# Performance work log

Measured on AMD Instinct MI355X. Metric: run time of the kernel, lower is better.

The kernel has to match this reference:

```python
import jax, jax.numpy as jnp
import numpy as np

C = 512
NUM_GROUPS = 32
EPS = 1e-6


def setup_inputs() -> dict:
    key = jax.random.key(0)
    ks = jax.random.split(key, 6)
    B, H, W = 4, 64, 64
    x = jax.random.normal(ks[0], (B, H, W, C), dtype=jnp.float32)
    # GroupNorm affine params (flax default init: scale=1, bias=0)
    gn_scale = jnp.ones((C,), jnp.float32)
    gn_bias = jnp.zeros((C,), jnp.float32)
    # 1x1 convs == per-pixel dense layers; weight [C_in, C_out], bias [C_out]
    def dense(k):
        return jax.random.normal(k, (C, C), dtype=jnp.float32) * 0.02
    wq, wk, wv, wo = dense(ks[1]), dense(ks[2]), dense(ks[3]), dense(ks[4])
    bq = jnp.zeros((C,), jnp.float32)
    bk = jnp.zeros((C,), jnp.float32)
    bv = jnp.zeros((C,), jnp.float32)
    bo = jnp.zeros((C,), jnp.float32)
    return {"x": x, "gn_scale": gn_scale, "gn_bias": gn_bias,
            "wq": wq, "bq": bq, "wk": wk, "bk": bk,
            "wv": wv, "bv": bv, "wo": wo, "bo": bo}


def _group_norm(x, scale, bias):
    B, H, W, Cc = x.shape
    g = NUM_GROUPS
    xg = x.reshape(B, H, W, g, Cc // g)
    mean = jnp.mean(xg, axis=(1, 2, 4), keepdims=True)
    var = jnp.var(xg, axis=(1, 2, 4), keepdims=True)
    xn = (xg - mean) * jax.lax.rsqrt(var + EPS)
    xn = xn.reshape(B, H, W, Cc)
    return xn * scale + bias


def reference(x, gn_scale, gn_bias, wq, bq, wk, bk, wv, bv, wo, bo):
    B, H, W, Cc = x.shape
    hn = _group_norm(x, gn_scale, gn_bias)
    # 1x1 convs
    q = (hn @ wq + bq).reshape(B, H * W, Cc)
    k = (hn @ wk + bk).reshape(B, H * W, Cc)
    v = (hn @ wv + bv).reshape(B, H * W, Cc)
    scale = jnp.asarray(Cc, x.dtype) ** -0.5
    # scores[b,i,j] = <q_i, k_j> * c^-0.5; softmax over keys j
    attn = jax.nn.softmax(jnp.einsum('bic,bjc->bij', q, k) * scale, axis=-1)
    out = jnp.einsum('bij,bjc->bic', attn, v).reshape(B, H, W, Cc)
    return x + (out @ wo + bo)
```

## Files before the change

### kernel.cpp

```cpp
#include <hip/hip_runtime.h>


typedef __attribute__((ext_vector_type(8))) __bf16 bf16x8;
typedef __attribute__((ext_vector_type(4))) __bf16 bf16x4;
typedef __attribute__((ext_vector_type(4))) float  floatx4;

#define C_DIM 512
#define SPB   4096
#define MTOT  16384

#define HN_OFF  ((size_t)0)
#define Q_OFF   ((size_t)16 << 20)
#define K_OFF   ((size_t)32 << 20)
#define V4_OFF  ((size_t)48 << 20)
#define WT_OFF  ((size_t)64 << 20)
#define O1_OFF  ((size_t)68 << 20)
#define ML_OFF  ((size_t)84 << 20)
#define GS_OFF  (ML_OFF + (size_t)(256 << 10))

__device__ inline floatx4 mfma16(bf16x8 a, bf16x8 b, floatx4 c) {
    return __builtin_amdgcn_mfma_f32_16x16x32_bf16(a, b, c, 0, 0, 0);
}

__device__ inline void gload16(const void* g, void* lds) {
    __builtin_amdgcn_global_load_lds(
        (const __attribute__((address_space(1))) unsigned int*)g,
        (__attribute__((address_space(3))) unsigned int*)lds, 16, 0, 0);
}

__global__ __launch_bounds__(256) void zero_stats(float* gstats) {
    gstats[threadIdx.x] = 0.f;
}

__global__ __launch_bounds__(256) void gn_stats(
    const float* __restrict__ x, float* __restrict__ gstats) {
    int bg = blockIdx.x;
    int b = bg >> 5, g = bg & 31;
    int tid = threadIdx.x;
    int cq = tid & 3, s0 = tid >> 2;
    const float* base = x + (size_t)b * SPB * C_DIM + g * 16 + cq * 4
                          + (size_t)blockIdx.y * 1024 * C_DIM;
    float sum = 0.f, sq = 0.f;
#pragma unroll 4
    for (int i = 0; i < 16; ++i) {
        floatx4 v = *(const floatx4*)(base + (size_t)(i * 64 + s0) * C_DIM);
        sum += v[0] + v[1] + v[2] + v[3];
        sq  += v[0]*v[0] + v[1]*v[1] + v[2]*v[2] + v[3]*v[3];
    }
#pragma unroll
    for (int off = 1; off < 64; off <<= 1) {
        sum += __shfl_xor(sum, off);
        sq  += __shfl_xor(sq,  off);
    }
    __shared__ float sm[8];
    int w = tid >> 6, lane = tid & 63;
    if (lane == 0) { sm[w] = sum; sm[4 + w] = sq; }
    __syncthreads();
    if (tid == 0) {
        atomicAdd(&gstats[bg * 2],     sm[0] + sm[1] + sm[2] + sm[3]);
        atomicAdd(&gstats[bg * 2 + 1], sm[4] + sm[5] + sm[6] + sm[7]);
    }
}

__global__ __launch_bounds__(256) void gn_apply(
    const float* __restrict__ x, const float* __restrict__ gstats,
    const float* __restrict__ gsc, const float* __restrict__ gbi,
    __bf16* __restrict__ hn) {
    int bg = blockIdx.x;
    int b = bg >> 5, g = bg & 31;
    int tid = threadIdx.x;
    int cq = tid & 3, s0 = tid >> 2;
    float S  = gstats[bg * 2], Qs = gstats[bg * 2 + 1];
    float mean = S * (1.f / 65536.f);
    float var  = Qs * (1.f / 65536.f) - mean * mean;
    float rstd = rsqrtf(var + 1e-6f);
    float sc[4], bi[4];
#pragma unroll
    for (int j = 0; j < 4; ++j) {
        float s_ = gsc[g * 16 + cq * 4 + j] * rstd;
        sc[j] = s_;
        bi[j] = gbi[g * 16 + cq * 4 + j] - mean * s_;
    }
    size_t off = (size_t)b * SPB * C_DIM + g * 16 + cq * 4
               + (size_t)blockIdx.y * 1024 * C_DIM;
    const float* base = x + off;
    __bf16* hbase = hn + off;
#pragma unroll 4
    for (int i = 0; i < 16; ++i) {
        floatx4 v = *(const floatx4*)(base + (size_t)(i * 64 + s0) * C_DIM);
        bf16x4 o;
#pragma unroll
        for (int j = 0; j < 4; ++j) o[j] = (__bf16)(v[j] * sc[j] + bi[j]);
        *(bf16x4*)(hbase + (size_t)(i * 64 + s0) * C_DIM) = o;
    }
}

__global__ __launch_bounds__(256) void wt_kernel(
    const float* __restrict__ w0, const float* __restrict__ w1,
    const float* __restrict__ w2, const float* __restrict__ w3,
    __bf16* __restrict__ wt) {
    const float* srcs[4] = {w0, w1, w2, w3};
    const float* src = srcs[blockIdx.z];
    __bf16* dst = wt + (size_t)blockIdx.z * C_DIM * C_DIM;
    __shared__ float tile[32][33];
    int tx = threadIdx.x & 31, ty = threadIdx.x >> 5;
    int gx = blockIdx.x * 32, gy = blockIdx.y * 32;
#pragma unroll
    for (int i = 0; i < 4; ++i)
        tile[ty + i * 8][tx] = src[(size_t)(gy + ty + i * 8) * C_DIM + gx + tx];
    __syncthreads();
#pragma unroll
    for (int i = 0; i < 4; ++i) {
        int n = gx + ty + i * 8;
        int k = gy + tx;
        dst[(size_t)n * C_DIM + k] = (__bf16)tile[tx][ty + i * 8];
    }
}

__global__ __launch_bounds__(256, 2) void proj_qkv(
    const __bf16* __restrict__ hn, const __bf16* __restrict__ wt_all,
    const float* __restrict__ bq, const float* __restrict__ bk,
    const float* __restrict__ bv, __bf16* __restrict__ qout,
    __bf16* __restrict__ kout, __bf16* __restrict__ v4out) {
    int z = blockIdx.z;
    const __bf16* wt = wt_all + (size_t)z * C_DIM * C_DIM;
    const float* bias = (z == 0) ? bq : (z == 1) ? bk : bv;
    __shared__ __bf16 Alds[128 * 32];
    __shared__ __bf16 Blds[128 * 32];
    int tid = threadIdx.x, lane = tid & 63, w = tid >> 6;
    int c = lane & 15, quad = lane >> 4;
    int wm = w & 1, wn = w >> 1;
    int mbase = blockIdx.x * 128, nbase = blockIdx.y * 128;
    floatx4 acc[4][4] = {};
    for (int kb = 0; kb < 16; ++kb) {
        __syncthreads();
#pragma unroll
        for (int p = 0; p < 2; ++p) {
            int chunk0 = w * 128 + p * 64;
            int chunk = chunk0 + lane;
            int row = chunk >> 2, qk = chunk & 3;
            gload16(hn + (size_t)(mbase + row) * C_DIM + kb * 32 + qk * 8, Alds + chunk0 * 8);
            gload16(wt + (size_t)(nbase + row) * C_DIM + kb * 32 + qk * 8, Blds + chunk0 * 8);
        }
        __syncthreads();
        bf16x8 af[4], bfr[4];
#pragma unroll
        for (int mt = 0; mt < 4; ++mt)
            af[mt] = *(const bf16x8*)(Alds + (wm * 64 + mt * 16 + c) * 32 + quad * 8);
#pragma unroll
        for (int nt = 0; nt < 4; ++nt)
            bfr[nt] = *(const bf16x8*)(Blds + (wn * 64 + nt * 16 + c) * 32 + quad * 8);
#pragma unroll
        for (int mt = 0; mt < 4; ++mt)
#pragma unroll
            for (int nt = 0; nt < 4; ++nt)
                acc[mt][nt] = mfma16(af[mt], bfr[nt], acc[mt][nt]);
    }
    float scale = (z == 0) ? 0.0441941738241592f : 1.0f;
#pragma unroll
    for (int nt = 0; nt < 4; ++nt) {
        int n = nbase + wn * 64 + nt * 16 + c;
        float bval = bias[n];
#pragma unroll
        for (int mt = 0; mt < 4; ++mt) {
            int m0 = mbase + wm * 64 + mt * 16 + quad * 4;
#pragma unroll
            for (int r = 0; r < 4; ++r) {
                int m = m0 + r;
                float val = (acc[mt][nt][r] + bval) * scale;
                if (z == 0)      qout[(size_t)m * C_DIM + n] = (__bf16)val;
                else if (z == 1) kout[(size_t)m * C_DIM + n] = (__bf16)val;
                else {
                    int bb = m >> 12, pos = m & 4095;
                    v4out[((size_t)(bb * 512 + (pos >> 3)) * C_DIM + n) * 8 + (pos & 7)] = (__bf16)val;
                }
            }
        }
    }
}

__device__ inline void stage_K(const __bf16* kbase, int key0,
                               __bf16* Klds, int w, int lane) {
#pragma unroll
    for (int p = 0; p < 8; ++p) {
        int chunk0 = w * 512 + p * 64;
        int chunk = chunk0 + lane;
        gload16(kbase + (size_t)(key0 + (chunk & 31)) * C_DIM + (chunk >> 5) * 8,
                Klds + chunk0 * 8);
    }
}

__device__ inline void stage_V(const __bf16* vsrc, __bf16* Vlds, int w, int lane) {
#pragma unroll
    for (int p = 0; p < 8; ++p) {
        int chunk0 = w * 512 + p * 64;
        gload16(vsrc + (size_t)(chunk0 + lane) * 8, Vlds + chunk0 * 8);
    }
}

__global__ __launch_bounds__(256, 2) void flash_kernel(
    const __bf16* __restrict__ q, const __bf16* __restrict__ kmat,
    const __bf16* __restrict__ v4, __bf16* __restrict__ op0,
    __bf16* __restrict__ op1, float* __restrict__ lpart) {
    __shared__ __bf16 Klds[16384];
    __shared__ __bf16 Vlds[16384];
    __shared__ __bf16 Plds[64 * 40];
    int tid = threadIdx.x, lane = tid & 63, w = tid >> 6;
    int c = lane & 15, quad = lane >> 4;
    int bid = blockIdx.x;
    int xcd = bid & 7;
    int b = xcd >> 1, h = xcd & 1, qt = bid >> 3;

    const __bf16* qp = q + ((size_t)(b * SPB + qt * 64 + w * 16 + c)) * C_DIM + quad * 8;
    bf16x8 qf[16];
#pragma unroll
    for (int ks = 0; ks < 16; ++ks) qf[ks] = *(const bf16x8*)(qp + ks * 32);
    floatx4 o[4][8];
#pragma unroll
    for (int mg = 0; mg < 4; ++mg)
#pragma unroll
        for (int t = 0; t < 8; ++t) o[mg][t] = (floatx4){0.f, 0.f, 0.f, 0.f};
    float l_r[4] = {0.f, 0.f, 0.f, 0.f};

    const __bf16* kbase = kmat + (size_t)b * SPB * C_DIM;
    const __bf16* vbase = v4 + (size_t)b * 512 * C_DIM * 8;

    stage_K(kbase, h * 2048, Klds, w, lane);
    __syncthreads();

    for (int kt = 0; kt < 64; ++kt) {
        int key0 = h * 2048 + kt * 32;
        stage_V(vbase + (size_t)(key0 >> 3) * C_DIM * 8, Vlds, w, lane);
        floatx4 s0 = (floatx4){0.f,0.f,0.f,0.f}, s1 = (floatx4){0.f,0.f,0.f,0.f};
#pragma unroll
        for (int ks = 0; ks < 16; ++ks) {
            bf16x8 k0 = *(const bf16x8*)(Klds + (((ks * 4 + quad) * 32) + c) * 8);
            bf16x8 k1 = *(const bf16x8*)(Klds + (((ks * 4 + quad) * 32) + c + 16) * 8);
            s0 = mfma16(qf[ks], k0, s0);
            s1 = mfma16(qf[ks], k1, s1);
        }
#pragma unroll
        for (int r = 0; r < 4; ++r) {
            float p0 = __expf(s0[r]);
            float p1 = __expf(s1[r]);
            l_r[r] += p0 + p1;
            int row = w * 16 + quad * 4 + r;
            Plds[row * 40 + c]      = (__bf16)p0;
            Plds[row * 40 + c + 16] = (__bf16)p1;
        }
        __syncthreads();
        int kn = (kt < 63) ? kt + 1 : 63;
        stage_K(kbase, h * 2048 + kn * 32, Klds, w, lane);
        bf16x8 pf[4];
#pragma unroll
        for (int mg = 0; mg < 4; ++mg)
            pf[mg] = *(const bf16x8*)(Plds + (mg * 16 + c) * 40 + quad * 8);
#pragma unroll
        for (int t = 0; t < 8; ++t) {
            bf16x8 vf = *(const bf16x8*)(Vlds + ((size_t)quad * 512 + w * 128 + t * 16 + c) * 8);
#pragma unroll
            for (int mg = 0; mg < 4; ++mg)
                o[mg][t] = mfma16(pf[mg], vf, o[mg][t]);
        }
        __syncthreads();
    }
#pragma unroll
    for (int r = 0; r < 4; ++r) {
        float l = l_r[r];
        l += __shfl_xor(l, 1);
        l += __shfl_xor(l, 2);
        l += __shfl_xor(l, 4);
        l += __shfl_xor(l, 8);
        l_r[r] = l;
    }
    if (c == 0) {
#pragma unroll
        for (int r = 0; r < 4; ++r) {
            int grow = b * SPB + qt * 64 + w * 16 + quad * 4 + r;
            lpart[h * MTOT + grow] = l_r[r];
        }
    }
    __bf16* ob = h ? op1 : op0;
#pragma unroll
    for (int mg = 0; mg < 4; ++mg)
#pragma unroll
        for (int t = 0; t < 8; ++t)
#pragma unroll
            for (int r = 0; r < 4; ++r) {
                int grow = b * SPB + qt * 64 + mg * 16 + quad * 4 + r;
                ob[(size_t)grow * C_DIM + w * 128 + t * 16 + c] = (__bf16)o[mg][t][r];
            }
}

__global__ __launch_bounds__(256) void combine_kernel(
    const __bf16* __restrict__ o0, const __bf16* __restrict__ o1,
    const float* __restrict__ lpart, __bf16* __restrict__ attn) {
    int tid = threadIdx.x, lane = tid & 63, w = tid >> 6;
    int rbase = blockIdx.x * 64 + w * 16;
    for (int rr = 0; rr < 16; ++rr) {
        int row = rbase + rr;
        float inv = 1.f / (lpart[row] + lpart[MTOT + row]);
        bf16x8 v0 = *(const bf16x8*)(o0 + (size_t)row * C_DIM + lane * 8);
        bf16x8 v1 = *(const bf16x8*)(o1 + (size_t)row * C_DIM + lane * 8);
        bf16x8 r;
#pragma unroll
        for (int j = 0; j < 8; ++j) r[j] = (__bf16)(((float)v0[j] + (float)v1[j]) * inv);
        *(bf16x8*)(attn + (size_t)row * C_DIM + lane * 8) = r;
    }
}

__global__ __launch_bounds__(256, 2) void proj_out(
    const __bf16* __restrict__ attn, const __bf16* __restrict__ wot,
    const float* __restrict__ bo, const float* __restrict__ x,
    float* __restrict__ out) {
    __shared__ __bf16 Alds[128 * 32];
    __shared__ __bf16 Blds[128 * 32];
    int tid = threadIdx.x, lane = tid & 63, w = tid >> 6;
    int c = lane & 15, quad = lane >> 4;
    int wm = w & 1, wn = w >> 1;
    int mbase = blockIdx.x * 128, nbase = blockIdx.y * 128;
    floatx4 acc[4][4] = {};
    for (int kb = 0; kb < 16; ++kb) {
        __syncthreads();
#pragma unroll
        for (int p = 0; p < 2; ++p) {
            int chunk0 = w * 128 + p * 64;
            int chunk = chunk0 + lane;
            int row = chunk >> 2, qk = chunk & 3;
            gload16(attn + (size_t)(mbase + row) * C_DIM + kb * 32 + qk * 8, Alds + chunk0 * 8);
            gload16(wot + (size_t)(nbase + row) * C_DIM + kb * 32 + qk * 8, Blds + chunk0 * 8);
        }
        __syncthreads();
        bf16x8 af[4], bfr[4];
#pragma unroll
        for (int mt = 0; mt < 4; ++mt)
            af[mt] = *(const bf16x8*)(Alds + (wm * 64 + mt * 16 + c) * 32 + quad * 8);
#pragma unroll
        for (int nt = 0; nt < 4; ++nt)
            bfr[nt] = *(const bf16x8*)(Blds + (wn * 64 + nt * 16 + c) * 32 + quad * 8);
#pragma unroll
        for (int mt = 0; mt < 4; ++mt)
#pragma unroll
            for (int nt = 0; nt < 4; ++nt)
                acc[mt][nt] = mfma16(af[mt], bfr[nt], acc[mt][nt]);
    }
#pragma unroll
    for (int nt = 0; nt < 4; ++nt) {
        int n = nbase + wn * 64 + nt * 16 + c;
        float bval = bo[n];
#pragma unroll
        for (int mt = 0; mt < 4; ++mt) {
            int m0 = mbase + wm * 64 + mt * 16 + quad * 4;
#pragma unroll
            for (int r = 0; r < 4; ++r) {
                size_t idx = (size_t)(m0 + r) * C_DIM + n;
                out[idx] = acc[mt][nt][r] + bval + x[idx];
            }
        }
    }
}

extern "C" void kernel_launch(void* const* d_in, const int* in_sizes, int n_in,
                              void* d_out, int out_size, void* d_ws, size_t ws_size,
                              hipStream_t stream) {
    const float* x   = (const float*)d_in[0];
    const float* gsc = (const float*)d_in[1];
    const float* gbi = (const float*)d_in[2];
    const float* wq  = (const float*)d_in[3];
    const float* bq  = (const float*)d_in[4];
    const float* wk  = (const float*)d_in[5];
    const float* bk  = (const float*)d_in[6];
    const float* wv  = (const float*)d_in[7];
    const float* bv  = (const float*)d_in[8];
    const float* wo  = (const float*)d_in[9];
    const float* bo  = (const float*)d_in[10];
    char* ws = (char*)d_ws;
    __bf16* hn  = (__bf16*)(ws + HN_OFF);
    __bf16* qb  = (__bf16*)(ws + Q_OFF);
    __bf16* kb  = (__bf16*)(ws + K_OFF);
    __bf16* v4  = (__bf16*)(ws + V4_OFF);
    __bf16* wt  = (__bf16*)(ws + WT_OFF);
    __bf16* op0 = (__bf16*)(ws + HN_OFF);
    __bf16* op1 = (__bf16*)(ws + O1_OFF);
    float*  lp  = (float*)(ws + ML_OFF);
    float*  gs  = (float*)(ws + GS_OFF);
    __bf16* attn = qb;
    float* out = (float*)d_out;

    zero_stats<<<1, 256, 0, stream>>>(gs);
    wt_kernel<<<dim3(16, 16, 4), 256, 0, stream>>>(wq, wk, wv, wo, wt);
    gn_stats<<<dim3(128, 4), 256, 0, stream>>>(x, gs);
    gn_apply<<<dim3(128, 4), 256, 0, stream>>>(x, gs, gsc, gbi, hn);
    proj_qkv<<<dim3(128, 4, 3), 256, 0, stream>>>(hn, wt, bq, bk, bv, qb, kb, v4);
    flash_kernel<<<512, 256, 0, stream>>>(qb, kb, v4, op0, op1, lp);
    combine_kernel<<<256, 256, 0, stream>>>(op0, op1, lp, attn);
    proj_out<<<dim3(128, 4), 256, 0, stream>>>(attn, wt + (size_t)3 * C_DIM * C_DIM, bo, x, out);
}
```

Before: 433.7 us.

## Fuse split-KV combine into output projection and drop stats atomics

Removes the combine kernel by summing the two partial attention outputs while staging the A tile in proj_out, and applies the softmax row normalisation in the GEMM epilogue. Group-norm stats are written per slice and reduced in gn_apply, removing the zero kernel and atomics. This saves a launch and a full intermediate round trip, but proj_out now reads two buffers through registers instead of async LDS loads, which may reduce overlap.

```diff
diff --git a/kernel.cpp b/kernel.cpp
--- a/kernel.cpp
+++ b/kernel.cpp
@@ -26,10 +26,6 @@
     __builtin_amdgcn_global_load_lds(
         (const __attribute__((address_space(1))) unsigned int*)g,
         (__attribute__((address_space(3))) unsigned int*)lds, 16, 0, 0);
-}
-
-__global__ __launch_bounds__(256) void zero_stats(float* gstats) {
-    gstats[threadIdx.x] = 0.f;
 }
 
 __global__ __launch_bounds__(256) void gn_stats(
@@ -57,8 +53,8 @@
     if (lane == 0) { sm[w] = sum; sm[4 + w] = sq; }
     __syncthreads();
     if (tid == 0) {
-        atomicAdd(&gstats[bg * 2],     sm[0] + sm[1] + sm[2] + sm[3]);
-        atomicAdd(&gstats[bg * 2 + 1], sm[4] + sm[5] + sm[6] + sm[7]);
+        gstats[(bg * 4 + blockIdx.y) * 2]     = sm[0] + sm[1] + sm[2] + sm[3];
+        gstats[(bg * 4 + blockIdx.y) * 2 + 1] = sm[4] + sm[5] + sm[6] + sm[7];
     }
 }
 
@@ -70,7 +66,9 @@
     int b = bg >> 5, g = bg & 31;
     int tid = threadIdx.x;
     int cq = tid & 3, s0 = tid >> 2;
-    float S  = gstats[bg * 2], Qs = gstats[bg * 2 + 1];
+    const float* gsB = gstats + bg * 8;
+    float S  = gsB[0] + gsB[2] + gsB[4] + gsB[6];
+    float Qs = gsB[1] + gsB[3] + gsB[5] + gsB[7];
     float mean = S * (1.f / 65536.f);
     float var  = Qs * (1.f / 65536.f) - mean * mean;
     float rstd = rsqrtf(var + 1e-6f);
@@ -292,25 +290,9 @@
             }
 }
 
-__global__ __launch_bounds__(256) void combine_kernel(
+__global__ __launch_bounds__(256, 2) void proj_out(
     const __bf16* __restrict__ o0, const __bf16* __restrict__ o1,
-    const float* __restrict__ lpart, __bf16* __restrict__ attn) {
-    int tid = threadIdx.x, lane = tid & 63, w = tid >> 6;
-    int rbase = blockIdx.x * 64 + w * 16;
-    for (int rr = 0; rr < 16; ++rr) {
-        int row = rbase + rr;
-        float inv = 1.f / (lpart[row] + lpart[MTOT + row]);
-        bf16x8 v0 = *(const bf16x8*)(o0 + (size_t)row * C_DIM + lane * 8);
-        bf16x8 v1 = *(const bf16x8*)(o1 + (size_t)row * C_DIM + lane * 8);
-        bf16x8 r;
-#pragma unroll
-        for (int j = 0; j < 8; ++j) r[j] = (__bf16)(((float)v0[j] + (float)v1[j]) * inv);
-        *(bf16x8*)(attn + (size_t)row * C_DIM + lane * 8) = r;
-    }
-}
-
-__global__ __launch_bounds__(256, 2) void proj_out(
-    const __bf16* __restrict__ attn, const __bf16* __restrict__ wot,
+    const float* __restrict__ lpart, const __bf16* __restrict__ wot,
     const float* __restrict__ bo, const float* __restrict__ x,
     float* __restrict__ out) {
     __shared__ __bf16 Alds[128 * 32];
@@ -322,13 +304,25 @@
     floatx4 acc[4][4] = {};
     for (int kb = 0; kb < 16; ++kb) {
         __syncthreads();
+        bf16x8 a0[2], a1[2];
 #pragma unroll
         for (int p = 0; p < 2; ++p) {
-            int chunk0 = w * 128 + p * 64;
-            int chunk = chunk0 + lane;
+            int chunk = w * 128 + p * 64 + lane;
             int row = chunk >> 2, qk = chunk & 3;
-            gload16(attn + (size_t)(mbase + row) * C_DIM + kb * 32 + qk * 8, Alds + chunk0 * 8);
-            gload16(wot + (size_t)(nbase + row) * C_DIM + kb * 32 + qk * 8, Blds + chunk0 * 8);
+            size_t aoff = (size_t)(mbase + row) * C_DIM + kb * 32 + qk * 8;
+            a0[p] = *(const bf16x8*)(o0 + aoff);
+            a1[p] = *(const bf16x8*)(o1 + aoff);
+            gload16(wot + (size_t)(nbase + row) * C_DIM + kb * 32 + qk * 8,
+                    Blds + (w * 128 + p * 64) * 8);
+        }
+#pragma unroll
+        for (int p = 0; p < 2; ++p) {
+            int chunk = w * 128 + p * 64 + lane;
+            bf16x8 s;
+#pragma unroll
+            for (int j = 0; j < 8; ++j)
+                s[j] = (__bf16)((float)a0[p][j] + (float)a1[p][j]);
+            *(bf16x8*)(Alds + chunk * 8) = s;
         }
         __syncthreads();
         bf16x8 af[4], bfr[4];
@@ -344,6 +338,14 @@
             for (int nt = 0; nt < 4; ++nt)
                 acc[mt][nt] = mfma16(af[mt], bfr[nt], acc[mt][nt]);
     }
+    float inv[4][4];
+#pragma unroll
+    for (int mt = 0; mt < 4; ++mt)
+#pragma unroll
+        for (int r = 0; r < 4; ++r) {
+            int m = mbase + wm * 64 + mt * 16 + quad * 4 + r;
+            inv[mt][r] = 1.f / (lpart[m] + lpart[MTOT + m]);
+        }
 #pragma unroll
     for (int nt = 0; nt < 4; ++nt) {
         int n = nbase + wn * 64 + nt * 16 + c;
@@ -354,7 +356,7 @@
 #pragma unroll
             for (int r = 0; r < 4; ++r) {
                 size_t idx = (size_t)(m0 + r) * C_DIM + n;
-                out[idx] = acc[mt][nt][r] + bval + x[idx];
+                out[idx] = acc[mt][nt][r] * inv[mt][r] + bval + x[idx];
             }
         }
     }
@@ -384,15 +386,13 @@
     __bf16* op1 = (__bf16*)(ws + O1_OFF);
     float*  lp  = (float*)(ws + ML_OFF);
     float*  gs  = (float*)(ws + GS_OFF);
-    __bf16* attn = qb;
     float* out = (float*)d_out;
 
-    zero_stats<<<1, 256, 0, stream>>>(gs);
     wt_kernel<<<dim3(16, 16, 4), 256, 0, stream>>>(wq, wk, wv, wo, wt);
     gn_stats<<<dim3(128, 4), 256, 0, stream>>>(x, gs);
     gn_apply<<<dim3(128, 4), 256, 0, stream>>>(x, gs, gsc, gbi, hn);
     proj_qkv<<<dim3(128, 4, 3), 256, 0, stream>>>(hn, wt, bq, bk, bv, qb, kb, v4);
     flash_kernel<<<512, 256, 0, stream>>>(qb, kb, v4, op0, op1, lp);
-    combine_kernel<<<256, 256, 0, stream>>>(op0, op1, lp, attn);
-    proj_out<<<dim3(128, 4), 256, 0, stream>>>(attn, wt + (size_t)3 * C_DIM * C_DIM, bo, x, out);
-}
+    proj_out<<<dim3(128, 4), 256, 0, stream>>>(op0, op1, lp,
+        wt + (size_t)3 * C_DIM * C_DIM, bo, x, out);
+}
```

Result: faster. 415.3 us (-4.2%).
